# Optimization experiments

Hardware: AMD Instinct MI355X
Metric: run time of the kernel (lower is better)

The kernel has to match this reference:

```python
import jax, jax.numpy as jnp
import numpy as np

D_MODEL = 768
N_HEADS = 12
D_K = D_MODEL // N_HEADS


def setup_inputs() -> dict:
    key = jax.random.key(0)
    ks = jax.random.split(key, 9)
    s = 1.0 / np.sqrt(D_MODEL)
    return {
        "x": jax.random.normal(ks[0], (2, 2048, D_MODEL), dtype=jnp.float32),
        "w_q": jax.random.normal(ks[1], (D_MODEL, D_MODEL), dtype=jnp.float32) * s,
        "b_q": jax.random.normal(ks[2], (D_MODEL,), dtype=jnp.float32) * 0.02,
        "w_k": jax.random.normal(ks[3], (D_MODEL, D_MODEL), dtype=jnp.float32) * s,
        "b_k": jax.random.normal(ks[4], (D_MODEL,), dtype=jnp.float32) * 0.02,
        "w_v": jax.random.normal(ks[5], (D_MODEL, D_MODEL), dtype=jnp.float32) * s,
        "b_v": jax.random.normal(ks[6], (D_MODEL,), dtype=jnp.float32) * 0.02,
        "w_o": jax.random.normal(ks[7], (D_MODEL, D_MODEL), dtype=jnp.float32) * s,
        "b_o": jax.random.normal(ks[8], (D_MODEL,), dtype=jnp.float32) * 0.02,
    }


def reference(x, w_q, b_q, w_k, b_k, w_v, b_v, w_o, b_o):
    B, S, _ = x.shape
    # nn.Linear: y = x @ W^T + b
    def proj(w, b):
        y = jnp.einsum("bsd,ed->bse", x, w) + b
        # [B, S, D] -> [B, H, S, d_k]
        return y.reshape(B, S, N_HEADS, D_K).transpose(0, 2, 1, 3)

    q = proj(w_q, b_q)
    k = proj(w_k, b_k)
    v = proj(w_v, b_v)

    scale = 1.0 / np.sqrt(D_K).astype(np.float32)
    scores = jnp.einsum("bhqd,bhkd->bhqk", q, k) * scale  # [B,H,S,S]
    attn = jax.nn.softmax(scores, axis=-1)
    ctx = jnp.einsum("bhqk,bhkd->bhqd", attn, v)  # [B,H,S,d_k]
    ctx = ctx.transpose(0, 2, 1, 3).reshape(B, S, D_MODEL)
    out = jnp.einsum("bsd,ed->bse", ctx, w_o) + b_o
    return out
```

## Files before the change

### kernel.cpp

```cpp
#include <hip/hip_runtime.h>
#include <hip/hip_bf16.h>

#define B_   2
#define S_   2048
#define D_   768
#define H_   12
#define DK_  64
#define R_   (B_*S_)

typedef __attribute__((ext_vector_type(8))) short short8;
typedef __attribute__((ext_vector_type(4))) float f32x4;

__device__ __forceinline__ short f2b(float f) {
  union { float f; unsigned u; } x; x.f = f;
  unsigned r = x.u + 0x7fffu + ((x.u >> 16) & 1u);
  return (short)(r >> 16);
}

__device__ __forceinline__ void gl_lds16(const short* g, short* l) {
  __builtin_amdgcn_global_load_lds(
      (const __attribute__((address_space(1))) void*)g,
      (__attribute__((address_space(3))) void*)l, 16, 0, 0);
}

__global__ void cvt_kernel(const float* __restrict__ x,
                           const float* __restrict__ wq, const float* __restrict__ wk,
                           const float* __restrict__ wv, const float* __restrict__ wo,
                           short* __restrict__ xb, short* __restrict__ wb) {
  const int XQ = R_ * D_ / 4;
  const int WQ = D_ * D_ / 4;
  int idx = blockIdx.x * blockDim.x + threadIdx.x;
  const float* src; short* dst; int off;
  if (idx < XQ) { src = x; dst = xb; off = idx; }
  else {
    int wi = idx - XQ; int w = wi / WQ; off = wi - w * WQ;
    if      (w == 0) { src = wq; dst = wb; }
    else if (w == 1) { src = wk; dst = wb + D_*D_; }
    else if (w == 2) { src = wv; dst = wb + 2*D_*D_; }
    else             { src = wo; dst = wb + 3*D_*D_; }
  }
  float4 v = ((const float4*)src)[off];
  short4 o;
  o.x = f2b(v.x); o.y = f2b(v.y); o.z = f2b(v.z); o.w = f2b(v.w);
  ((short4*)dst)[off] = o;
}

__launch_bounds__(256)
__global__ void qkv_gemm_kernel(const short* __restrict__ xb, const short* __restrict__ wb,
                                const float* __restrict__ bq, const float* __restrict__ bk,
                                const float* __restrict__ bv,
                                short* __restrict__ Qw, short* __restrict__ Kw,
                                short* __restrict__ VTw) {
  __shared__ short As[128 * 32];
  __shared__ short Bs[128 * 32];
  const int which = blockIdx.z;
  const short* W = wb + which * (D_ * D_);
  const float* bias = (which == 0) ? bq : (which == 1) ? bk : bv;
  const int n0 = blockIdx.x * 128, m0 = blockIdx.y * 128;
  const int t = threadIdx.x, l = t & 63, w = t >> 6;
  const int wr = w >> 1, wc = w & 1;

  f32x4 acc[4][4] = {};

  const int srow = t >> 2, sseg = (t & 3) * 8;

  for (int k0 = 0; k0 < D_; k0 += 32) {
    __syncthreads();
    gl_lds16(xb + (m0 + srow) * D_ + k0 + sseg,      &As[t * 8]);
    gl_lds16(xb + (m0 + 64 + srow) * D_ + k0 + sseg, &As[(t + 256) * 8]);
    gl_lds16(W  + (n0 + srow) * D_ + k0 + sseg,      &Bs[t * 8]);
    gl_lds16(W  + (n0 + 64 + srow) * D_ + k0 + sseg, &Bs[(t + 256) * 8]);
    __syncthreads();
    short8 a[4], b[4];
#pragma unroll
    for (int i = 0; i < 4; i++)
      a[i] = *(const short8*)&As[(wr * 64 + i * 16 + (l & 15)) * 32 + (l >> 4) * 8];
#pragma unroll
    for (int i = 0; i < 4; i++)
      b[i] = *(const short8*)&Bs[(wc * 64 + i * 16 + (l & 15)) * 32 + (l >> 4) * 8];
#pragma unroll
    for (int i = 0; i < 4; i++)
#pragma unroll
      for (int j = 0; j < 4; j++)
        acc[i][j] = __builtin_amdgcn_mfma_f32_16x16x32_bf16(a[i], b[j], acc[i][j], 0, 0, 0);
  }

#pragma unroll
  for (int i = 0; i < 4; i++) {
#pragma unroll
    for (int j2 = 0; j2 < 4; j2++) {
      int mm = m0 + wr * 64 + i * 16 + (l >> 4) * 4 + j2;
      int bidx = mm >> 11, s = mm & 2047;
#pragma unroll
      for (int nj = 0; nj < 4; nj++) {
        int e = n0 + wc * 64 + nj * 16 + (l & 15);
        float val = acc[i][nj][j2] + bias[e];
        int h = e >> 6, dk = e & 63;
        int bh = bidx * H_ + h;
        if (which == 0)      Qw[(bh * S_ + s) * DK_ + dk] = f2b(val * 0.125f);
        else if (which == 1) Kw[(bh * S_ + s) * DK_ + dk] = f2b(val);
        else                 VTw[(bh * DK_ + dk) * S_ + s] = f2b(val);
      }
    }
  }
}

#define KVB 64
__launch_bounds__(256)
__global__ void attn_kernel(const short* __restrict__ Qw, const short* __restrict__ Kw,
                            const short* __restrict__ VTw, short* __restrict__ ctx) {
  __shared__ short Ksh[2][KVB * DK_];
  __shared__ short Vsh[2][DK_ * KVB];
  __shared__ short Psh[4][16 * 72];

  const int t = threadIdx.x, l = t & 63, w = t >> 6;
  const int bh = blockIdx.y;
  const int q0 = blockIdx.x * 64 + w * 16;
  const int bq = bh / H_, h = bh - bq * H_;
  const short* Qh = Qw + bh * S_ * DK_;
  const short* Kh = Kw + bh * S_ * DK_;
  const short* Vh = VTw + bh * DK_ * S_;
  short* pl = &Psh[w][0];

  const int i0 = t,        r0 = i0 >> 3, c0 = i0 & 7;
  const int i1 = t + 256,  r1 = i1 >> 3, c1 = i1 & 7;
  const int koff0 = r0 * DK_ + ((c0 ^ (r0 & 7)) << 3);
  const int koff1 = r1 * DK_ + ((c1 ^ (r1 & 7)) << 3);
  const int voff0 = r0 * S_  + ((c0 ^ (r0 & 7)) << 3);
  const int voff1 = r1 * S_  + ((c1 ^ (r1 & 7)) << 3);

#define STAGE(buf, kt) do { \
    gl_lds16(Kh + (kt) * DK_ + koff0, &Ksh[buf][i0 * 8]); \
    gl_lds16(Kh + (kt) * DK_ + koff1, &Ksh[buf][i1 * 8]); \
    gl_lds16(Vh + (kt) + voff0,       &Vsh[buf][i0 * 8]); \
    gl_lds16(Vh + (kt) + voff1,       &Vsh[buf][i1 * 8]); \
  } while (0)

  short8 qf[2];
#pragma unroll
  for (int ks = 0; ks < 2; ks++)
    qf[ks] = *(const short8*)&Qh[(q0 + (l & 15)) * DK_ + ks * 32 + (l >> 4) * 8];

  f32x4 acc_o[4] = {};
  float m_run = -INFINITY, l_run = 0.f;

  STAGE(0, 0);
  __syncthreads();
  int cur = 0;

  for (int kt = 0; kt < S_; kt += KVB) {
    if (kt + KVB < S_) STAGE(cur ^ 1, kt + KVB);

    f32x4 acc_s[4] = {};
    __builtin_amdgcn_s_setprio(1);
#pragma unroll
    for (int ni = 0; ni < 4; ni++) {
#pragma unroll
      for (int ks = 0; ks < 2; ks++) {
        int r = (l & 15) + 16 * ni;
        int cc = (l >> 4) + 4 * ks;
        short8 kf = *(const short8*)&Ksh[cur][r * DK_ + ((cc ^ (r & 7)) << 3)];
        acc_s[ni] = __builtin_amdgcn_mfma_f32_16x16x32_bf16(kf, qf[ks], acc_s[ni], 0, 0, 0);
      }
    }
    __builtin_amdgcn_s_setprio(0);

    float mx = -INFINITY;
#pragma unroll
    for (int ni = 0; ni < 4; ni++)
#pragma unroll
      for (int j = 0; j < 4; j++) mx = fmaxf(mx, acc_s[ni][j]);
    mx = fmaxf(mx, __shfl_xor(mx, 16));
    mx = fmaxf(mx, __shfl_xor(mx, 32));
    float mnew = fmaxf(m_run, mx);
    float fac = __expf(m_run - mnew);
    m_run = mnew;
    float sum = 0.f;
#pragma unroll
    for (int ni = 0; ni < 4; ni++)
#pragma unroll
      for (int j = 0; j < 4; j++) {
        float p = __expf(acc_s[ni][j] - mnew);
        acc_s[ni][j] = p;
        sum += p;
      }
    sum += __shfl_xor(sum, 16);
    sum += __shfl_xor(sum, 32);
    l_run = l_run * fac + sum;

    float facj[4];
#pragma unroll
    for (int j = 0; j < 4; j++) facj[j] = __shfl(fac, ((l >> 4) << 2) + j);
#pragma unroll
    for (int nd = 0; nd < 4; nd++)
#pragma unroll
      for (int j = 0; j < 4; j++) acc_o[nd][j] *= facj[j];

#pragma unroll
    for (int ni = 0; ni < 4; ni++) {
      short4 pk;
      pk.x = f2b(acc_s[ni][0]); pk.y = f2b(acc_s[ni][1]);
      pk.z = f2b(acc_s[ni][2]); pk.w = f2b(acc_s[ni][3]);
      *(short4*)&pl[(l & 15) * 72 + (l >> 4) * 4 + 16 * ni] = pk;
    }

    __builtin_amdgcn_s_setprio(1);
#pragma unroll
    for (int ks = 0; ks < 2; ks++) {
      short8 pa = *(const short8*)&pl[(l & 15) * 72 + (l >> 4) * 8 + 32 * ks];
#pragma unroll
      for (int nd = 0; nd < 4; nd++) {
        int r = (l & 15) + 16 * nd;
        int cc = (l >> 4) + 4 * ks;
        short8 vf = *(const short8*)&Vsh[cur][r * KVB + ((cc ^ (r & 7)) << 3)];
        acc_o[nd] = __builtin_amdgcn_mfma_f32_16x16x32_bf16(pa, vf, acc_o[nd], 0, 0, 0);
      }
    }
    __builtin_amdgcn_s_setprio(0);

    __syncthreads();
    cur ^= 1;
  }

  float inv = 1.f / l_run;
  float invj[4];
#pragma unroll
  for (int j = 0; j < 4; j++) invj[j] = __shfl(inv, ((l >> 4) << 2) + j);
#pragma unroll
  for (int nd = 0; nd < 4; nd++)
#pragma unroll
    for (int j = 0; j < 4; j++) {
      int s = q0 + (l >> 4) * 4 + j;
      ctx[(bq * S_ + s) * D_ + h * DK_ + (l & 15) + 16 * nd] = f2b(acc_o[nd][j] * invj[j]);
    }
#undef STAGE
}

__launch_bounds__(256)
__global__ void oproj_kernel(const short* __restrict__ ctx, const short* __restrict__ Wo,
                             const float* __restrict__ bo, float* __restrict__ out) {
  __shared__ short As[128 * 32];
  __shared__ short Bs[128 * 32];
  const int n0 = blockIdx.x * 128, m0 = blockIdx.y * 128;
  const int t = threadIdx.x, l = t & 63, w = t >> 6;
  const int wr = w >> 1, wc = w & 1;

  f32x4 acc[4][4] = {};
  const int srow = t >> 2, sseg = (t & 3) * 8;

  for (int k0 = 0; k0 < D_; k0 += 32) {
    __syncthreads();
    gl_lds16(ctx + (m0 + srow) * D_ + k0 + sseg,      &As[t * 8]);
    gl_lds16(ctx + (m0 + 64 + srow) * D_ + k0 + sseg, &As[(t + 256) * 8]);
    gl_lds16(Wo  + (n0 + srow) * D_ + k0 + sseg,      &Bs[t * 8]);
    gl_lds16(Wo  + (n0 + 64 + srow) * D_ + k0 + sseg, &Bs[(t + 256) * 8]);
    __syncthreads();
    short8 a[4], b[4];
#pragma unroll
    for (int i = 0; i < 4; i++)
      a[i] = *(const short8*)&As[(wr * 64 + i * 16 + (l & 15)) * 32 + (l >> 4) * 8];
#pragma unroll
    for (int i = 0; i < 4; i++)
      b[i] = *(const short8*)&Bs[(wc * 64 + i * 16 + (l & 15)) * 32 + (l >> 4) * 8];
#pragma unroll
    for (int i = 0; i < 4; i++)
#pragma unroll
      for (int j = 0; j < 4; j++)
        acc[i][j] = __builtin_amdgcn_mfma_f32_16x16x32_bf16(a[i], b[j], acc[i][j], 0, 0, 0);
  }

#pragma unroll
  for (int i = 0; i < 4; i++) {
#pragma unroll
    for (int j2 = 0; j2 < 4; j2++) {
      int mm = m0 + wr * 64 + i * 16 + (l >> 4) * 4 + j2;
#pragma unroll
      for (int nj = 0; nj < 4; nj++) {
        int e = n0 + wc * 64 + nj * 16 + (l & 15);
        out[mm * D_ + e] = acc[i][nj][j2] + bo[e];
      }
    }
  }
}

extern "C" void kernel_launch(void* const* d_in, const int* in_sizes, int n_in,
                              void* d_out, int out_size, void* d_ws, size_t ws_size,
                              hipStream_t stream) {
  (void)in_sizes; (void)n_in; (void)out_size; (void)ws_size;
  const float* x  = (const float*)d_in[0];
  const float* wq = (const float*)d_in[1];
  const float* bq = (const float*)d_in[2];
  const float* wk = (const float*)d_in[3];
  const float* bk = (const float*)d_in[4];
  const float* wv = (const float*)d_in[5];
  const float* bv = (const float*)d_in[6];
  const float* wo = (const float*)d_in[7];
  const float* bo = (const float*)d_in[8];
  float* out = (float*)d_out;

  short* xb  = (short*)d_ws;
  short* wb  = xb + R_ * D_;
  short* Qw  = wb + 4 * D_ * D_;
  short* Kw  = Qw + R_ * D_;
  short* VTw = Kw + R_ * D_;
  short* ctx = VTw + R_ * D_;

  cvt_kernel<<<5376, 256, 0, stream>>>(x, wq, wk, wv, wo, xb, wb);
  qkv_gemm_kernel<<<dim3(6, 32, 3), 256, 0, stream>>>(xb, wb, bq, bk, bv, Qw, Kw, VTw);
  attn_kernel<<<dim3(32, 24), 256, 0, stream>>>(Qw, Kw, VTw, ctx);
  oproj_kernel<<<dim3(6, 32), 256, 0, stream>>>(ctx, wb + 3 * D_ * D_, bo, out);
}
```

Baseline: 121.5 us.

## Give each attention wave 32 query rows, exp2 softmax with lazy rescaling

The attention kernel now runs 2 waves per block, each handling 32 query rows, so every K/V fragment read from LDS feeds two MFMAs. The log2(e) factor is folded into the Q scaling so softmax can use the native exp2. The running-max rescale of the output accumulators is skipped unless some row's max grows by more than a threshold, which relies on fp32 headroom. Probabilities are packed with the hardware bf16 pack instruction. In exchange each wave holds more registers and each block has fewer threads to issue the staging loads.

```diff
diff --git a/kernel.cpp b/kernel.cpp
--- a/kernel.cpp
+++ b/kernel.cpp
@@ -7,6 +7,7 @@
 #define H_   12
 #define DK_  64
 #define R_   (B_*S_)
+#define LOG2E_OVER8 0.18033688011112042f
 
 typedef __attribute__((ext_vector_type(8))) short short8;
 typedef __attribute__((ext_vector_type(4))) float f32x4;
@@ -15,6 +16,12 @@
   union { float f; unsigned u; } x; x.f = f;
   unsigned r = x.u + 0x7fffu + ((x.u >> 16) & 1u);
   return (short)(r >> 16);
+}
+
+__device__ __forceinline__ unsigned cvt_pk_bf16(float lo, float hi) {
+  unsigned r;
+  asm("v_cvt_pk_bf16_f32 %0, %1, %2" : "=v"(r) : "v"(lo), "v"(hi));
+  return r;
 }
 
 __device__ __forceinline__ void gl_lds16(const short* g, short* l) {
@@ -97,7 +104,7 @@
         float val = acc[i][nj][j2] + bias[e];
         int h = e >> 6, dk = e & 63;
         int bh = bidx * H_ + h;
-        if (which == 0)      Qw[(bh * S_ + s) * DK_ + dk] = f2b(val * 0.125f);
+        if (which == 0)      Qw[(bh * S_ + s) * DK_ + dk] = f2b(val * LOG2E_OVER8);
         else if (which == 1) Kw[(bh * S_ + s) * DK_ + dk] = f2b(val);
         else                 VTw[(bh * DK_ + dk) * S_ + s] = f2b(val);
       }
@@ -106,43 +113,44 @@
 }
 
 #define KVB 64
-__launch_bounds__(256)
+__launch_bounds__(128)
 __global__ void attn_kernel(const short* __restrict__ Qw, const short* __restrict__ Kw,
                             const short* __restrict__ VTw, short* __restrict__ ctx) {
   __shared__ short Ksh[2][KVB * DK_];
   __shared__ short Vsh[2][DK_ * KVB];
-  __shared__ short Psh[4][16 * 72];
+  __shared__ short Psh[2][32 * 72];
 
   const int t = threadIdx.x, l = t & 63, w = t >> 6;
   const int bh = blockIdx.y;
-  const int q0 = blockIdx.x * 64 + w * 16;
+  const int q0 = blockIdx.x * 64 + w * 32;
   const int bq = bh / H_, h = bh - bq * H_;
   const short* Qh = Qw + bh * S_ * DK_;
   const short* Kh = Kw + bh * S_ * DK_;
   const short* Vh = VTw + bh * DK_ * S_;
   short* pl = &Psh[w][0];
 
-  const int i0 = t,        r0 = i0 >> 3, c0 = i0 & 7;
-  const int i1 = t + 256,  r1 = i1 >> 3, c1 = i1 & 7;
+  const int r0 = t >> 3, c0 = t & 7;
   const int koff0 = r0 * DK_ + ((c0 ^ (r0 & 7)) << 3);
-  const int koff1 = r1 * DK_ + ((c1 ^ (r1 & 7)) << 3);
   const int voff0 = r0 * S_  + ((c0 ^ (r0 & 7)) << 3);
-  const int voff1 = r1 * S_  + ((c1 ^ (r1 & 7)) << 3);
 
 #define STAGE(buf, kt) do { \
-    gl_lds16(Kh + (kt) * DK_ + koff0, &Ksh[buf][i0 * 8]); \
-    gl_lds16(Kh + (kt) * DK_ + koff1, &Ksh[buf][i1 * 8]); \
-    gl_lds16(Vh + (kt) + voff0,       &Vsh[buf][i0 * 8]); \
-    gl_lds16(Vh + (kt) + voff1,       &Vsh[buf][i1 * 8]); \
+    _Pragma("unroll") \
+    for (int j = 0; j < 4; j++) { \
+      gl_lds16(Kh + (kt) * DK_ + koff0 + 1024 * j,  &Ksh[buf][t * 8 + 1024 * j]); \
+      gl_lds16(Vh + (kt) + voff0 + 16 * S_ * j,     &Vsh[buf][t * 8 + 1024 * j]); \
+    } \
   } while (0)
 
-  short8 qf[2];
-#pragma unroll
-  for (int ks = 0; ks < 2; ks++)
-    qf[ks] = *(const short8*)&Qh[(q0 + (l & 15)) * DK_ + ks * 32 + (l >> 4) * 8];
-
-  f32x4 acc_o[4] = {};
-  float m_run = -INFINITY, l_run = 0.f;
+  short8 qf[2][2];
+#pragma unroll
+  for (int mi = 0; mi < 2; mi++)
+#pragma unroll
+    for (int ks = 0; ks < 2; ks++)
+      qf[mi][ks] = *(const short8*)&Qh[(q0 + 16 * mi + (l & 15)) * DK_ + ks * 32 + (l >> 4) * 8];
+
+  f32x4 acc_o[2][4] = {};
+  float m_run[2] = {-3.0e38f, -3.0e38f};
+  float l_run[2] = {0.f, 0.f};
 
   STAGE(0, 0);
   __syncthreads();
@@ -151,69 +159,85 @@
   for (int kt = 0; kt < S_; kt += KVB) {
     if (kt + KVB < S_) STAGE(cur ^ 1, kt + KVB);
 
-    f32x4 acc_s[4] = {};
+    f32x4 acc_s[2][4] = {};
     __builtin_amdgcn_s_setprio(1);
 #pragma unroll
     for (int ni = 0; ni < 4; ni++) {
+      int r = (l & 15) + 16 * ni;
 #pragma unroll
       for (int ks = 0; ks < 2; ks++) {
-        int r = (l & 15) + 16 * ni;
         int cc = (l >> 4) + 4 * ks;
         short8 kf = *(const short8*)&Ksh[cur][r * DK_ + ((cc ^ (r & 7)) << 3)];
-        acc_s[ni] = __builtin_amdgcn_mfma_f32_16x16x32_bf16(kf, qf[ks], acc_s[ni], 0, 0, 0);
+        acc_s[0][ni] = __builtin_amdgcn_mfma_f32_16x16x32_bf16(kf, qf[0][ks], acc_s[0][ni], 0, 0, 0);
+        acc_s[1][ni] = __builtin_amdgcn_mfma_f32_16x16x32_bf16(kf, qf[1][ks], acc_s[1][ni], 0, 0, 0);
       }
     }
     __builtin_amdgcn_s_setprio(0);
 
-    float mx = -INFINITY;
-#pragma unroll
-    for (int ni = 0; ni < 4; ni++)
-#pragma unroll
-      for (int j = 0; j < 4; j++) mx = fmaxf(mx, acc_s[ni][j]);
-    mx = fmaxf(mx, __shfl_xor(mx, 16));
-    mx = fmaxf(mx, __shfl_xor(mx, 32));
-    float mnew = fmaxf(m_run, mx);
-    float fac = __expf(m_run - mnew);
-    m_run = mnew;
-    float sum = 0.f;
-#pragma unroll
-    for (int ni = 0; ni < 4; ni++)
-#pragma unroll
-      for (int j = 0; j < 4; j++) {
-        float p = __expf(acc_s[ni][j] - mnew);
-        acc_s[ni][j] = p;
-        sum += p;
-      }
-    sum += __shfl_xor(sum, 16);
-    sum += __shfl_xor(sum, 32);
-    l_run = l_run * fac + sum;
-
-    float facj[4];
-#pragma unroll
-    for (int j = 0; j < 4; j++) facj[j] = __shfl(fac, ((l >> 4) << 2) + j);
-#pragma unroll
-    for (int nd = 0; nd < 4; nd++)
-#pragma unroll
-      for (int j = 0; j < 4; j++) acc_o[nd][j] *= facj[j];
-
-#pragma unroll
-    for (int ni = 0; ni < 4; ni++) {
-      short4 pk;
-      pk.x = f2b(acc_s[ni][0]); pk.y = f2b(acc_s[ni][1]);
-      pk.z = f2b(acc_s[ni][2]); pk.w = f2b(acc_s[ni][3]);
-      *(short4*)&pl[(l & 15) * 72 + (l >> 4) * 4 + 16 * ni] = pk;
+    float mx[2];
+#pragma unroll
+    for (int mi = 0; mi < 2; mi++) {
+      float m = -3.0e38f;
+#pragma unroll
+      for (int ni = 0; ni < 4; ni++)
+#pragma unroll
+        for (int j = 0; j < 4; j++) m = fmaxf(m, acc_s[mi][ni][j]);
+      m = fmaxf(m, __shfl_xor(m, 16));
+      m = fmaxf(m, __shfl_xor(m, 32));
+      mx[mi] = m;
+    }
+    float dm = fmaxf(mx[0] - m_run[0], mx[1] - m_run[1]);
+    if (!__all(dm <= 11.5f)) {
+#pragma unroll
+      for (int mi = 0; mi < 2; mi++) {
+        float mnew = fmaxf(m_run[mi], mx[mi]);
+        float fac = __builtin_amdgcn_exp2f(m_run[mi] - mnew);
+        m_run[mi] = mnew;
+        l_run[mi] *= fac;
+        float fj[4];
+#pragma unroll
+        for (int j = 0; j < 4; j++) fj[j] = __shfl(fac, ((l >> 4) << 2) + j);
+#pragma unroll
+        for (int nd = 0; nd < 4; nd++)
+#pragma unroll
+          for (int j = 0; j < 4; j++) acc_o[mi][nd][j] *= fj[j];
+      }
+    }
+#pragma unroll
+    for (int mi = 0; mi < 2; mi++) {
+      float sum = 0.f;
+#pragma unroll
+      for (int ni = 0; ni < 4; ni++)
+#pragma unroll
+        for (int j = 0; j < 4; j++) {
+          float p = __builtin_amdgcn_exp2f(acc_s[mi][ni][j] - m_run[mi]);
+          acc_s[mi][ni][j] = p;
+          sum += p;
+        }
+      sum += __shfl_xor(sum, 16);
+      sum += __shfl_xor(sum, 32);
+      l_run[mi] += sum;
+#pragma unroll
+      for (int ni = 0; ni < 4; ni++) {
+        uint2 pw;
+        pw.x = cvt_pk_bf16(acc_s[mi][ni][0], acc_s[mi][ni][1]);
+        pw.y = cvt_pk_bf16(acc_s[mi][ni][2], acc_s[mi][ni][3]);
+        *(uint2*)&pl[(16 * mi + (l & 15)) * 72 + (l >> 4) * 4 + 16 * ni] = pw;
+      }
     }
 
     __builtin_amdgcn_s_setprio(1);
 #pragma unroll
     for (int ks = 0; ks < 2; ks++) {
-      short8 pa = *(const short8*)&pl[(l & 15) * 72 + (l >> 4) * 8 + 32 * ks];
+      short8 pa0 = *(const short8*)&pl[(l & 15) * 72 + (l >> 4) * 8 + 32 * ks];
+      short8 pa1 = *(const short8*)&pl[(16 + (l & 15)) * 72 + (l >> 4) * 8 + 32 * ks];
 #pragma unroll
       for (int nd = 0; nd < 4; nd++) {
         int r = (l & 15) + 16 * nd;
         int cc = (l >> 4) + 4 * ks;
         short8 vf = *(const short8*)&Vsh[cur][r * KVB + ((cc ^ (r & 7)) << 3)];
-        acc_o[nd] = __builtin_amdgcn_mfma_f32_16x16x32_bf16(pa, vf, acc_o[nd], 0, 0, 0);
+        acc_o[0][nd] = __builtin_amdgcn_mfma_f32_16x16x32_bf16(pa0, vf, acc_o[0][nd], 0, 0, 0);
+        acc_o[1][nd] = __builtin_amdgcn_mfma_f32_16x16x32_bf16(pa1, vf, acc_o[1][nd], 0, 0, 0);
       }
     }
     __builtin_amdgcn_s_setprio(0);
@@ -222,17 +246,20 @@
     cur ^= 1;
   }
 
-  float inv = 1.f / l_run;
-  float invj[4];
-#pragma unroll
-  for (int j = 0; j < 4; j++) invj[j] = __shfl(inv, ((l >> 4) << 2) + j);
-#pragma unroll
-  for (int nd = 0; nd < 4; nd++)
-#pragma unroll
-    for (int j = 0; j < 4; j++) {
-      int s = q0 + (l >> 4) * 4 + j;
-      ctx[(bq * S_ + s) * D_ + h * DK_ + (l & 15) + 16 * nd] = f2b(acc_o[nd][j] * invj[j]);
-    }
+#pragma unroll
+  for (int mi = 0; mi < 2; mi++) {
+    float inv = 1.f / l_run[mi];
+    float invj[4];
+#pragma unroll
+    for (int j = 0; j < 4; j++) invj[j] = __shfl(inv, ((l >> 4) << 2) + j);
+#pragma unroll
+    for (int nd = 0; nd < 4; nd++)
+#pragma unroll
+      for (int j = 0; j < 4; j++) {
+        int s = q0 + 16 * mi + (l >> 4) * 4 + j;
+        ctx[(bq * S_ + s) * D_ + h * DK_ + (l & 15) + 16 * nd] = f2b(acc_o[mi][nd][j] * invj[j]);
+      }
+  }
 #undef STAGE
 }
 
@@ -307,6 +334,6 @@
 
   cvt_kernel<<<5376, 256, 0, stream>>>(x, wq, wk, wv, wo, xb, wb);
   qkv_gemm_kernel<<<dim3(6, 32, 3), 256, 0, stream>>>(xb, wb, bq, bk, bv, Qw, Kw, VTw);
-  attn_kernel<<<dim3(32, 24), 256, 0, stream>>>(Qw, Kw, VTw, ctx);
+  attn_kernel<<<dim3(32, 24), 128, 0, stream>>>(Qw, Kw, VTw, ctx);
   oproj_kernel<<<dim3(6, 32), 256, 0, stream>>>(ctx, wb + 3 * D_ * D_, bo, out);
 }
```

Result: slower. 124.3 us (+2.3%).
